# Kernel tuning notes

Measured on AMD Instinct MI355X. Metric: run time of the kernel, lower is better.

Reference implementation:

```python
import jax, jax.numpy as jnp
import numpy as np

GRID = (32, 32, 32)
LOWER = jnp.array([0.0, 0.0, 0.0], jnp.float32)
UPPER = jnp.array([1.0, 1.0, 1.0], jnp.float32)
B = 16
N = 131072
C_IN = 1018          # per-point feature channels; +3 offset +3 xyz = 1024 = nn_channels[0]
D_IN = 1024
C_OUT = 128          # nn_channels[-1]
BN_EPS = 1e-5


def setup_inputs() -> dict:
    key = jax.random.key(0)
    ks = jax.random.split(key, 8)
    W1 = jax.random.normal(ks[5], (D_IN, C_OUT), jnp.float32) / np.sqrt(D_IN).astype(np.float32)
    return {
        "xyz": jax.random.uniform(ks[0], (N, 3), jnp.float32),
        "pred_nocs": jax.random.uniform(ks[1], (N, 3), jnp.float32),
        "per_point_features": jax.random.normal(ks[2], (N, C_IN), jnp.float32),
        "pred_confidence": jax.random.uniform(ks[3], (N, 1), jnp.float32),
        "batch_idx": jnp.sort(jax.random.randint(ks[4], (N,), 0, B, dtype=jnp.int32)),
        "batch_size": B,
        "W1": W1,
        "b1": jnp.zeros((C_OUT,), jnp.float32),
        "g1": jnp.ones((C_OUT,), jnp.float32),
        "be1": jnp.zeros((C_OUT,), jnp.float32),
    }


def _batchnorm_train(x, gamma, beta):
    # torch BatchNorm1d in training mode: biased variance over the batch dim
    m = jnp.mean(x, axis=0)
    v = jnp.mean(jnp.square(x - m), axis=0)
    return (x - m) * jax.lax.rsqrt(v + BN_EPS) * gamma + beta


def reference(xyz, pred_nocs, per_point_features, pred_confidence, batch_idx,
              batch_size, W1, b1, g1, be1):
    gs_f = jnp.array(GRID, jnp.float32)
    gs_i = jnp.array(GRID, jnp.int32)
    # VirtualGrid.get_points_grid_idxs: round to nearest cell, clip into grid
    idx_f = jnp.round((pred_nocs - LOWER) / (UPPER - LOWER) * (gs_f - 1.0))
    idx = jnp.clip(idx_f.astype(jnp.int32), 0, gs_i - 1)  # [N,3]
    # VirtualGrid.idxs_to_points
    grid_pts = idx.astype(jnp.float32) / (gs_f - 1.0) * (UPPER - LOWER) + LOWER
    local_offset = pred_nocs - grid_pts
    feats = jnp.concatenate([per_point_features, local_offset, xyz], axis=-1)  # [N,1024]
    # local_nn: Linear -> ReLU -> PointBatchNorm1D
    h = _batchnorm_train(jax.nn.relu(feats @ W1 + b1), g1, be1)  # [N,128]
    # flatten (b,i,j,k) -> flat grid index
    gx, gy, gz = GRID
    flat = ((batch_idx.astype(jnp.int32) * gx + idx[:, 0]) * gy + idx[:, 1]) * gz + idx[:, 2]
    num_grids = batch_size * gx * gy * gz
    ssum = jax.ops.segment_sum(h, flat, num_segments=num_grids)          # [num_grids,128]
    cnt = jax.ops.segment_sum(jnp.ones((h.shape[0], 1), h.dtype), flat, num_segments=num_grids)
    mean = ssum / jnp.maximum(cnt, 1.0)  # empty cells stay 0 (torch_scatter mean)
    # [num_grids, C] -> [B, gx, gy, gz, C] -> [B, C, gx, gy, gz]
    vol = mean.reshape(batch_size, gx, gy, gz, C_OUT).transpose(0, 4, 1, 2, 3)
    return vol
```

## Files before the change

kernel.cpp:

```cpp
#include <hip/hip_runtime.h>

#define NPTS   131072
#define CIN    1018
#define DIN    1024
#define COUT   128
#define BB     16
#define GDIM   32
#define NCELLS (BB*GDIM*GDIM*GDIM)
#define NREP   8

typedef float          f32x4  __attribute__((ext_vector_type(4)));
typedef __bf16         bf16x8 __attribute__((ext_vector_type(8)));
typedef unsigned short us8    __attribute__((ext_vector_type(8)));

__device__ __forceinline__ unsigned short f2bf(float f) {
    union { float f; unsigned u; } v; v.f = f;
    unsigned r = v.u + 0x7FFFu + ((v.u >> 16) & 1u);
    return (unsigned short)(r >> 16);
}

__device__ __forceinline__ us8 cvt8f(f32x4 lo, f32x4 hi) {
    bf16x8 r;
    r[0] = (__bf16)lo[0]; r[1] = (__bf16)lo[1]; r[2] = (__bf16)lo[2]; r[3] = (__bf16)lo[3];
    r[4] = (__bf16)hi[0]; r[5] = (__bf16)hi[1]; r[6] = (__bf16)hi[2]; r[7] = (__bf16)hi[3];
    return __builtin_bit_cast(us8, r);
}

__device__ __forceinline__ f32x4 MF(us8 a, us8 b, f32x4 c) {
    return __builtin_amdgcn_mfma_f32_16x16x32_bf16(
        __builtin_bit_cast(bf16x8, a), __builtin_bit_cast(bf16x8, b), c, 0, 0, 0);
}

__global__ __launch_bounds__(256) void k_zero(int4* __restrict__ p, int n4) {
    const int idx = blockIdx.x * 256 + threadIdx.x;
    const int4 z = {0, 0, 0, 0};
    for (int i = idx; i < n4; i += 131072) p[i] = z;
}

__global__ __launch_bounds__(256) void k_packW(const float* __restrict__ W1,
                                               unsigned short* __restrict__ pw) {
    const int t  = blockIdx.x * 256 + threadIdx.x;
    const int l  = t & 63;
    const int cb = (t >> 6) & 7;
    const int ks = t >> 9;
    const int col  = cb * 16 + (l & 15);
    const int krow = ks * 32 + ((l >> 4) * 8);
    unsigned short* dst = pw + (size_t)t * 8;
#pragma unroll
    for (int i = 0; i < 8; ++i) dst[i] = f2bf(W1[(size_t)(krow + i) * COUT + col]);
}

__global__ __launch_bounds__(256) void k_prep(const float* __restrict__ xyz,
                                              const float* __restrict__ nocs,
                                              const float* __restrict__ feats,
                                              const int*   __restrict__ bidx,
                                              float* __restrict__ tail,
                                              int*   __restrict__ cellid,
                                              int*   __restrict__ cnt) {
    const int i = blockIdx.x * 256 + threadIdx.x;
    if (i >= NPTS) return;
    int id[3]; float off[3];
#pragma unroll
    for (int d = 0; d < 3; ++d) {
        const float nv = nocs[i * 3 + d];
        int ii = (int)rintf(nv * 31.0f);
        ii = ii < 0 ? 0 : (ii > 31 ? 31 : ii);
        id[d]  = ii;
        off[d] = nv - (float)ii / 31.0f;
    }
    float* tl = tail + (size_t)i * 8;
    tl[0] = feats[(size_t)i * CIN + 1016];
    tl[1] = feats[(size_t)i * CIN + 1017];
    tl[2] = off[0]; tl[3] = off[1]; tl[4] = off[2];
    tl[5] = xyz[i*3+0]; tl[6] = xyz[i*3+1]; tl[7] = xyz[i*3+2];
    const int cell = ((bidx[i] * GDIM + id[0]) * GDIM + id[1]) * GDIM + id[2];
    cellid[i] = cell;
    atomicAdd(&cnt[cell], 1);
}

__global__ __launch_bounds__(256) void k_scanA(const int* __restrict__ cnt,
                                               int* __restrict__ rel,
                                               int* __restrict__ bsum) {
    __shared__ int wtot[4], woff[4];
    const int t = threadIdx.x, blk = blockIdx.x;
    const int4 c4 = *(const int4*)&cnt[blk * 1024 + t * 4];
    const int s = c4.x + c4.y + c4.z + c4.w;
    int v = s;
    const int lane = t & 63, w = t >> 6;
#pragma unroll
    for (int d = 1; d < 64; d <<= 1) {
        const int u = __shfl_up(v, d);
        if (lane >= d) v += u;
    }
    if (lane == 63) wtot[w] = v;
    __syncthreads();
    if (t == 0) {
        int a = 0;
#pragma unroll
        for (int i = 0; i < 4; ++i) { woff[i] = a; a += wtot[i]; }
        bsum[blk] = a;
    }
    __syncthreads();
    const int excl = woff[w] + v - s;
    int* r = rel + blk * 1024 + t * 4;
    r[0] = excl; r[1] = excl + c4.x;
    r[2] = excl + c4.x + c4.y; r[3] = excl + c4.x + c4.y + c4.z;
}

__global__ __launch_bounds__(256) void k_scanB(const int* __restrict__ bsum,
                                               int* __restrict__ boff) {
    __shared__ int wtot[4], woff[4];
    const int t = threadIdx.x;
    const int2 c2 = *(const int2*)&bsum[t * 2];
    const int s = c2.x + c2.y;
    int v = s;
    const int lane = t & 63, w = t >> 6;
#pragma unroll
    for (int d = 1; d < 64; d <<= 1) {
        const int u = __shfl_up(v, d);
        if (lane >= d) v += u;
    }
    if (lane == 63) wtot[w] = v;
    __syncthreads();
    if (t == 0) {
        int a = 0;
#pragma unroll
        for (int i = 0; i < 4; ++i) { woff[i] = a; a += wtot[i]; }
    }
    __syncthreads();
    const int excl = woff[w] + v - s;
    boff[t * 2] = excl; boff[t * 2 + 1] = excl + c2.x;
}

__global__ __launch_bounds__(256) void k_fill(const int* __restrict__ cellid,
                                              const int* __restrict__ rel,
                                              const int* __restrict__ boff,
                                              int* __restrict__ cursor,
                                              int* __restrict__ dstrow) {
    const int i = blockIdx.x * 256 + threadIdx.x;
    if (i >= NPTS) return;
    const int cell = cellid[i];
    const int slot = atomicAdd(&cursor[cell], 1);
    dstrow[i] = rel[cell] + boff[cell >> 10] + slot;
}


template<int DIRECT>
__global__ void k_gemm(const float* __restrict__ feats,
                       const float* __restrict__ tail,
                       const int*   __restrict__ dstrow,
                       const float* __restrict__ b1,
                       const unsigned short* __restrict__ pw,
                       float* __restrict__ dst,
                       float* __restrict__ gstats) {
    __shared__ float S[3 * 12288];
    const int t = threadIdx.x;
    const int w = t >> 6, l = t & 63;
    const int kgrp = l >> 4, l15 = l & 15;
    const int row0b = blockIdx.x * 128;
    const int swz = l15 & 7;
    const int lr = w * 16 + l15;

    f32x4 acc[8];
#pragma unroll
    for (int cb = 0; cb < 8; ++cb) {
#pragma unroll
        for (int d = 0; d < 4; ++d) acc[cb][d] = 0.f;
    }

#define STAGE6(stg, ch) do{                                               \
    float* _base = S + (stg) * 12288;                                     \
    _Pragma("unroll")                                                     \
    for (int _i = 0; _i < 4; ++_i) {            \
        const int _s   = t + _i * 512;                                    \
        const int _row = _s >> 4;                                         \
        const int _c4  = (_s & 15) ^ (_row & 7);                          \
        const int _k   = (ch) * 64 + _c4 * 4;                             \
        const float* _src = (_k < 1016)                                   \
            ? feats + (size_t)(row0b + _row) * CIN + _k                   \
            : tail  + (size_t)(row0b + _row) * 8 + (_k - 1016);           \
        __builtin_amdgcn_global_load_lds(                                 \
            (const __attribute__((address_space(1))) void*)_src,          \
            (__attribute__((address_space(3))) void*)&_base[_s * 4],      \
            16, 0, 0);                                                    \
    }                                                                     \
    _Pragma("unroll")                                                     \
    for (int _i = 0; _i < 2; ++_i) {            \
        const int _s = t + _i * 512;                                      \
        __builtin_amdgcn_global_load_lds(                                 \
            (const __attribute__((address_space(1))) void*)                \
                (pw + (size_t)(ch) * 8192 + (size_t)_s * 8),              \
            (__attribute__((address_space(3))) void*)&_base[8192 + _s*4], \
            16, 0, 0);                                                    \
    }                                                                     \
}while(0)

    STAGE6(0, 0);
    STAGE6(1, 1);
    int cur = 0, nxt2 = 2;
    for (int ch = 0; ch < 16; ++ch) {
        __builtin_amdgcn_sched_barrier(0);
        if (ch == 15) asm volatile("s_waitcnt vmcnt(0)" ::: "memory");
        else          asm volatile("s_waitcnt vmcnt(6)" ::: "memory");
        __builtin_amdgcn_sched_barrier(0);
        __builtin_amdgcn_s_barrier();
        __builtin_amdgcn_sched_barrier(0);
        if (ch + 2 < 16) STAGE6(nxt2, ch + 2);
        const float* bufA = S + cur * 12288;
        const unsigned short* bufB = (const unsigned short*)(bufA + 8192);
#pragma unroll
        for (int ks = 0; ks < 2; ++ks) {
            const int c4a = ks * 8 + kgrp * 2;
            const f32x4 lo = *(const f32x4*)&bufA[lr * 64 + (( c4a      ^ swz) << 2)];
            const f32x4 hi = *(const f32x4*)&bufA[lr * 64 + (((c4a + 1) ^ swz) << 2)];
            const us8 a = cvt8f(lo, hi);
#pragma unroll
            for (int cb = 0; cb < 8; ++cb) {
                const us8 b = *(const us8*)(bufB + (((ks * 8 + cb) * 64) + l) * 8);
                acc[cb] = MF(a, b, acc[cb]);
            }
        }
        __builtin_amdgcn_sched_barrier(0);
        cur  = cur  == 2 ? 0 : cur + 1;
        nxt2 = nxt2 == 2 ? 0 : nxt2 + 1;
    }
#undef STAGE6

    int r0[4];
#pragma unroll
    for (int j = 0; j < 4; ++j)
        r0[j] = dstrow[row0b + w * 16 + kgrp * 4 + j];
    float* grep = gstats + (size_t)((blockIdx.x * 8 + w) & (NREP - 1)) * 256;
#pragma unroll
    for (int cb = 0; cb < 8; ++cb) {
        const int c = cb * 16 + l15;
        const float bias = b1[c];
        float s = 0.f, q = 0.f;
#pragma unroll
        for (int j = 0; j < 4; ++j) {
            float v0 = acc[cb][j] + bias; v0 = v0 > 0.f ? v0 : 0.f;
            if (DIRECT) {
                const int a = r0[j];
                unsafeAtomicAdd(dst + (((size_t)((a >> 15) * COUT + c)) << 15) + (a & 32767), v0);
            } else {
                dst[(size_t)r0[j] * COUT + c] = v0;
            }
            s += v0; q += v0 * v0;
        }
        s += __shfl_xor(s, 16); s += __shfl_xor(s, 32);
        q += __shfl_xor(q, 16); q += __shfl_xor(q, 32);
        if (l < 16) {
            unsafeAtomicAdd(grep + c, s);
            unsafeAtomicAdd(grep + COUT + c, q);
        }
    }
}

__global__ void k_stats(const float* __restrict__ gstats, const float* __restrict__ g1,
                        const float* __restrict__ be1, float* __restrict__ ss) {
    const int c = threadIdx.x;
    float sm = 0.f, sq = 0.f;
#pragma unroll
    for (int r = 0; r < NREP; ++r) {
        sm += gstats[r * 256 + c];
        sq += gstats[r * 256 + COUT + c];
    }
    const float invn = 1.0f / (float)NPTS;
    const float mean = sm * invn;
    float var = sq * invn - mean * mean;
    var = var < 0.f ? 0.f : var;
    const float sc = g1[c] * rsqrtf(var + 1e-5f);
    ss[c] = sc;
    ss[COUT + c] = be1[c] - mean * sc;
}

__global__ __launch_bounds__(256) void k_out(const float* __restrict__ h,
                                             const int* __restrict__ cnt,
                                             const int* __restrict__ rel,
                                             const int* __restrict__ boff,
                                             const float* __restrict__ ss,
                                             float* __restrict__ out) {
    __shared__ float tile[128 * 128];
    __shared__ float linv[128];
    __shared__ float lss[256];
    const int t  = threadIdx.x;
    const int s0 = blockIdx.x * 128;
    const int b = s0 >> 15, sp0 = s0 & 32767;
    const int boff0 = boff[s0 >> 10];
    if (t < 128) {
        const int cn = cnt[s0 + t];
        linv[t] = cn > 0 ? 1.0f / (float)cn : 0.f;
    } else {
        const int c = t - 128;
        lss[c] = ss[c]; lss[128 + c] = ss[COUT + c];
    }
    const int q = t & 31, r8 = t >> 5;
#pragma unroll
    for (int rep = 0; rep < 16; ++rep) {
        const int j = r8 + rep * 8;
        const int cj = cnt[s0 + j];
        if (cj > 0) {
            const int st = rel[s0 + j] + boff0;
            f32x4 v; v[0] = v[1] = v[2] = v[3] = 0.f;
            for (int k = 0; k < cj; ++k) {
                const f32x4 hv = *(const f32x4*)&h[(size_t)(st + k) * COUT + q * 4];
                v[0] += hv[0]; v[1] += hv[1]; v[2] += hv[2]; v[3] += hv[3];
            }
#pragma unroll
            for (int d = 0; d < 4; ++d) {
                const int c = q * 4 + d;
                tile[c * 128 + (j ^ (c & 28))] = v[d];
            }
        }
    }
    __syncthreads();
#pragma unroll
    for (int p = 0; p < 16; ++p) {
        const int c = p * 8 + r8;
        const float sc = lss[c], sh = lss[128 + c];
        const int u = c & 28;
        const f32x4 vv = *(const f32x4*)&tile[c * 128 + ((q * 4) ^ u)];
        f32x4 o;
#pragma unroll
        for (int d = 0; d < 4; ++d) {
            const float inv = linv[q * 4 + d];
            o[d] = inv > 0.f ? vv[d] * inv * sc + sh : 0.f;
        }
        *(f32x4*)&out[(((size_t)(b * COUT + c)) << 15) + sp0 + q * 4] = o;
    }
}

__global__ __launch_bounds__(256) void k_norm_inplace(float* __restrict__ out,
                                                      const int* __restrict__ cnt,
                                                      const float* __restrict__ ss,
                                                      size_t total) {
    const size_t i = ((size_t)blockIdx.x * 256 + threadIdx.x) * 4;
    if (i >= total) return;
    const int c = (int)((i >> 15) & 127);
    const size_t cellb = ((i >> 22) << 15) | (i & 32767);
    f32x4 v = *(f32x4*)&out[i];
    const int4 cn = *(const int4*)&cnt[cellb];
    const float sc = ss[c], sh = ss[COUT + c];
    const int cna[4] = {cn.x, cn.y, cn.z, cn.w};
#pragma unroll
    for (int d = 0; d < 4; ++d)
        v[d] = cna[d] > 0 ? v[d] / (float)cna[d] * sc + sh : 0.f;
    *(f32x4*)&out[i] = v;
}

extern "C" void kernel_launch(void* const* d_in, const int* in_sizes, int n_in,
                              void* d_out, int out_size, void* d_ws, size_t ws_size,
                              hipStream_t stream) {
    const float* xyz   = (const float*)d_in[0];
    const float* nocs  = (const float*)d_in[1];
    const float* feats = (const float*)d_in[2];
    const int*   bidx  = (const int*)d_in[4];
    const float* W1    = (const float*)d_in[6];
    const float* b1    = (const float*)d_in[7];
    const float* g1    = (const float*)d_in[8];
    const float* be1   = (const float*)d_in[9];
    float* out = (float*)d_out;
    float* ws  = (float*)d_ws;

    const size_t HF  = (size_t)NPTS * COUT;
    const size_t STF = NREP * 256;
    const size_t oA_h    = 0;
    const size_t oA_cnt  = HF;
    const size_t oA_cur  = oA_cnt + NCELLS;
    const size_t oA_st   = oA_cur + NCELLS;
    const size_t oA_rel  = oA_st + STF;
    const size_t oA_bof  = oA_rel + NCELLS;
    const size_t oA_dr   = oA_bof + 512;
    const size_t oA_ss   = oA_dr + NPTS;
    const size_t oA_tail = oA_ss + 256;
    const size_t oA_cid  = oA_tail + (size_t)NPTS * 8;
    const size_t oA_pw   = oA_cid + NPTS;
    const size_t needA   = (oA_pw + 65536) * sizeof(float);
    const bool planA = ws_size >= needA;

    const size_t oB_cnt = 0, oB_st = NCELLS, oB_ss = oB_st + STF,
                 oB_tail = oB_ss + 256, oB_cid = oB_tail + (size_t)NPTS * 8,
                 oB_pw = oB_cid + NPTS;

    float* h   = planA ? ws + oA_h : nullptr;
    int*   cnt = (int*)(ws + (planA ? oA_cnt : oB_cnt));
    int*   cur = planA ? (int*)(ws + oA_cur) : nullptr;
    float* st  = ws + (planA ? oA_st : oB_st);
    int*   rel = planA ? (int*)(ws + oA_rel) : nullptr;
    int*   bof = planA ? (int*)(ws + oA_bof) : nullptr;
    int*   dr  = planA ? (int*)(ws + oA_dr) : nullptr;
    float* ssb = ws + (planA ? oA_ss : oB_ss);
    float* tl  = ws + (planA ? oA_tail : oB_tail);
    int*   cid = (int*)(ws + (planA ? oA_cid : oB_cid));
    unsigned short* pw = (unsigned short*)(ws + (planA ? oA_pw : oB_pw));

    if (planA) {
        k_zero<<<512, 256, 0, stream>>>((int4*)cnt, (int)((2 * NCELLS + STF) / 4));
    } else {
        k_zero<<<512, 256, 0, stream>>>((int4*)cnt, (int)((NCELLS + STF) / 4));
        hipMemsetAsync(out, 0, (size_t)out_size * sizeof(float), stream);
    }

    k_packW<<<64, 256, 0, stream>>>(W1, pw);
    k_prep<<<NPTS / 256, 256, 0, stream>>>(xyz, nocs, feats, bidx, tl, cid, cnt);
    if (planA) {
        k_scanA<<<512, 256, 0, stream>>>(cnt, rel, bof);
        k_scanB<<<1, 256, 0, stream>>>(bof, bof);
        k_fill<<<NPTS / 256, 256, 0, stream>>>(cid, rel, bof, cur, dr);
        k_gemm<0><<<NPTS / 128, 512, 0, stream>>>(feats, tl, dr, b1, pw, h, st);
        k_stats<<<1, 128, 0, stream>>>(st, g1, be1, ssb);
        k_out<<<NCELLS / 128, 256, 0, stream>>>(h, cnt, rel, bof, ssb, out);
    } else {
        k_gemm<1><<<NPTS / 128, 512, 0, stream>>>(feats, tl, cid, b1, pw, out, st);
        k_stats<<<1, 128, 0, stream>>>(st, g1, be1, ssb);
        const size_t total = (size_t)out_size;
        k_norm_inplace<<<(unsigned)((total + 1023) / 1024), 256, 0, stream>>>(out, cnt, ssb, total);
    }
    (void)in_sizes; (void)n_in; (void)d_in;
}
```

Baseline: 346.6 us.

## Merge small launches, fold BN stats into output kernel, remap block order

Merges the weight-pack and zeroing kernels into one launch, moves cursor zeroing into the scan kernel, and folds the BN statistics reduction into each block of the output kernel so the single-block stats launch disappears. The GEMM and output kernels now use an XCD-aware block index remap. The output kernel is reshaped to 64 cells per block with a padded shared-memory tile instead of an XOR swizzle, which lowers LDS use and raises occupancy. The goal is less launch overhead and better cache locality, at the cost of every output block recomputing the stats reduction.

```diff
diff --git a/kernel.cpp b/kernel.cpp
--- a/kernel.cpp
+++ b/kernel.cpp
@@ -31,23 +31,25 @@
         __builtin_bit_cast(bf16x8, a), __builtin_bit_cast(bf16x8, b), c, 0, 0, 0);
 }
 
-__global__ __launch_bounds__(256) void k_zero(int4* __restrict__ p, int n4) {
-    const int idx = blockIdx.x * 256 + threadIdx.x;
-    const int4 z = {0, 0, 0, 0};
-    for (int i = idx; i < n4; i += 131072) p[i] = z;
-}
-
-__global__ __launch_bounds__(256) void k_packW(const float* __restrict__ W1,
-                                               unsigned short* __restrict__ pw) {
-    const int t  = blockIdx.x * 256 + threadIdx.x;
-    const int l  = t & 63;
-    const int cb = (t >> 6) & 7;
-    const int ks = t >> 9;
-    const int col  = cb * 16 + (l & 15);
-    const int krow = ks * 32 + ((l >> 4) * 8);
-    unsigned short* dst = pw + (size_t)t * 8;
-#pragma unroll
-    for (int i = 0; i < 8; ++i) dst[i] = f2bf(W1[(size_t)(krow + i) * COUT + col]);
+__global__ __launch_bounds__(256) void k_zp(const float* __restrict__ W1,
+                                            unsigned short* __restrict__ pw,
+                                            int4* __restrict__ zp, int n4) {
+    const int t = threadIdx.x;
+    if (blockIdx.x < 64) {
+        const int g  = blockIdx.x * 256 + t;
+        const int l  = g & 63;
+        const int cb = (g >> 6) & 7;
+        const int ks = g >> 9;
+        const int col  = cb * 16 + (l & 15);
+        const int krow = ks * 32 + ((l >> 4) * 8);
+        unsigned short* dst = pw + (size_t)g * 8;
+#pragma unroll
+        for (int i = 0; i < 8; ++i) dst[i] = f2bf(W1[(size_t)(krow + i) * COUT + col]);
+    } else {
+        const int idx = (blockIdx.x - 64) * 256 + t;
+        const int4 z = {0, 0, 0, 0};
+        for (int i = idx; i < n4; i += 512 * 256) zp[i] = z;
+    }
 }
 
 __global__ __launch_bounds__(256) void k_prep(const float* __restrict__ xyz,
@@ -80,9 +82,12 @@
 
 __global__ __launch_bounds__(256) void k_scanA(const int* __restrict__ cnt,
                                                int* __restrict__ rel,
-                                               int* __restrict__ bsum) {
+                                               int* __restrict__ bsum,
+                                               int4* __restrict__ cursor) {
     __shared__ int wtot[4], woff[4];
     const int t = threadIdx.x, blk = blockIdx.x;
+    const int4 z = {0, 0, 0, 0};
+    cursor[blk * 256 + t] = z;
     const int4 c4 = *(const int4*)&cnt[blk * 1024 + t * 4];
     const int s = c4.x + c4.y + c4.z + c4.w;
     int v = s;
@@ -157,7 +162,8 @@
     const int t = threadIdx.x;
     const int w = t >> 6, l = t & 63;
     const int kgrp = l >> 4, l15 = l & 15;
-    const int row0b = blockIdx.x * 128;
+    const int lb = (blockIdx.x & 7) * ((int)gridDim.x >> 3) + (blockIdx.x >> 3);
+    const int row0b = lb * 128;
     const int swz = l15 & 7;
     const int lr = w * 16 + l15;
 
@@ -278,25 +284,40 @@
                                              const int* __restrict__ cnt,
                                              const int* __restrict__ rel,
                                              const int* __restrict__ boff,
-                                             const float* __restrict__ ss,
+                                             const float* __restrict__ gstats,
+                                             const float* __restrict__ g1,
+                                             const float* __restrict__ be1,
                                              float* __restrict__ out) {
-    __shared__ float tile[128 * 128];
-    __shared__ float linv[128];
+    __shared__ float tile[128 * 68];
+    __shared__ float linv[64];
     __shared__ float lss[256];
     const int t  = threadIdx.x;
-    const int s0 = blockIdx.x * 128;
+    const int lb = (blockIdx.x & 7) * ((int)gridDim.x >> 3) + (blockIdx.x >> 3);
+    const int s0 = lb * 64;
     const int b = s0 >> 15, sp0 = s0 & 32767;
     const int boff0 = boff[s0 >> 10];
-    if (t < 128) {
+    if (t < 64) {
         const int cn = cnt[s0 + t];
         linv[t] = cn > 0 ? 1.0f / (float)cn : 0.f;
-    } else {
+    } else if (t >= 128) {
         const int c = t - 128;
-        lss[c] = ss[c]; lss[128 + c] = ss[COUT + c];
+        float sm = 0.f, sq = 0.f;
+#pragma unroll
+        for (int r = 0; r < NREP; ++r) {
+            sm += gstats[r * 256 + c];
+            sq += gstats[r * 256 + COUT + c];
+        }
+        const float invn = 1.0f / (float)NPTS;
+        const float mean = sm * invn;
+        float var = sq * invn - mean * mean;
+        var = var < 0.f ? 0.f : var;
+        const float sc = g1[c] * rsqrtf(var + 1e-5f);
+        lss[c] = sc;
+        lss[128 + c] = be1[c] - mean * sc;
     }
     const int q = t & 31, r8 = t >> 5;
 #pragma unroll
-    for (int rep = 0; rep < 16; ++rep) {
+    for (int rep = 0; rep < 8; ++rep) {
         const int j = r8 + rep * 8;
         const int cj = cnt[s0 + j];
         if (cj > 0) {
@@ -307,26 +328,23 @@
                 v[0] += hv[0]; v[1] += hv[1]; v[2] += hv[2]; v[3] += hv[3];
             }
 #pragma unroll
-            for (int d = 0; d < 4; ++d) {
-                const int c = q * 4 + d;
-                tile[c * 128 + (j ^ (c & 28))] = v[d];
-            }
+            for (int d = 0; d < 4; ++d) tile[(q * 4 + d) * 68 + j] = v[d];
         }
     }
     __syncthreads();
-#pragma unroll
-    for (int p = 0; p < 16; ++p) {
-        const int c = p * 8 + r8;
+    const int qq = t & 15, rr = t >> 4;
+#pragma unroll
+    for (int p = 0; p < 8; ++p) {
+        const int c = p * 16 + rr;
         const float sc = lss[c], sh = lss[128 + c];
-        const int u = c & 28;
-        const f32x4 vv = *(const f32x4*)&tile[c * 128 + ((q * 4) ^ u)];
+        const f32x4 vv = *(const f32x4*)&tile[c * 68 + qq * 4];
         f32x4 o;
 #pragma unroll
         for (int d = 0; d < 4; ++d) {
-            const float inv = linv[q * 4 + d];
+            const float inv = linv[qq * 4 + d];
             o[d] = inv > 0.f ? vv[d] * inv * sc + sh : 0.f;
         }
-        *(f32x4*)&out[(((size_t)(b * COUT + c)) << 15) + sp0 + q * 4] = o;
+        *(f32x4*)&out[(((size_t)(b * COUT + c)) << 15) + sp0 + qq * 4] = o;
     }
 }
 
@@ -366,9 +384,9 @@
     const size_t STF = NREP * 256;
     const size_t oA_h    = 0;
     const size_t oA_cnt  = HF;
-    const size_t oA_cur  = oA_cnt + NCELLS;
-    const size_t oA_st   = oA_cur + NCELLS;
-    const size_t oA_rel  = oA_st + STF;
+    const size_t oA_st   = oA_cnt + NCELLS;
+    const size_t oA_cur  = oA_st + STF;
+    const size_t oA_rel  = oA_cur + NCELLS;
     const size_t oA_bof  = oA_rel + NCELLS;
     const size_t oA_dr   = oA_bof + 512;
     const size_t oA_ss   = oA_dr + NPTS;
@@ -384,8 +402,8 @@
 
     float* h   = planA ? ws + oA_h : nullptr;
     int*   cnt = (int*)(ws + (planA ? oA_cnt : oB_cnt));
+    float* st  = ws + (planA ? oA_st : oB_st);
     int*   cur = planA ? (int*)(ws + oA_cur) : nullptr;
-    float* st  = ws + (planA ? oA_st : oB_st);
     int*   rel = planA ? (int*)(ws + oA_rel) : nullptr;
     int*   bof = planA ? (int*)(ws + oA_bof) : nullptr;
     int*   dr  = planA ? (int*)(ws + oA_dr) : nullptr;
@@ -394,22 +412,16 @@
     int*   cid = (int*)(ws + (planA ? oA_cid : oB_cid));
     unsigned short* pw = (unsigned short*)(ws + (planA ? oA_pw : oB_pw));
 
-    if (planA) {
-        k_zero<<<512, 256, 0, stream>>>((int4*)cnt, (int)((2 * NCELLS + STF) / 4));
-    } else {
-        k_zero<<<512, 256, 0, stream>>>((int4*)cnt, (int)((NCELLS + STF) / 4));
-        hipMemsetAsync(out, 0, (size_t)out_size * sizeof(float), stream);
-    }
-
-    k_packW<<<64, 256, 0, stream>>>(W1, pw);
+    k_zp<<<576, 256, 0, stream>>>(W1, pw, (int4*)cnt, (int)((NCELLS + STF) / 4));
+    if (!planA) hipMemsetAsync(out, 0, (size_t)out_size * sizeof(float), stream);
+
     k_prep<<<NPTS / 256, 256, 0, stream>>>(xyz, nocs, feats, bidx, tl, cid, cnt);
     if (planA) {
-        k_scanA<<<512, 256, 0, stream>>>(cnt, rel, bof);
+        k_scanA<<<512, 256, 0, stream>>>(cnt, rel, bof, (int4*)cur);
         k_scanB<<<1, 256, 0, stream>>>(bof, bof);
         k_fill<<<NPTS / 256, 256, 0, stream>>>(cid, rel, bof, cur, dr);
         k_gemm<0><<<NPTS / 128, 512, 0, stream>>>(feats, tl, dr, b1, pw, h, st);
-        k_stats<<<1, 128, 0, stream>>>(st, g1, be1, ssb);
-        k_out<<<NCELLS / 128, 256, 0, stream>>>(h, cnt, rel, bof, ssb, out);
+        k_out<<<NCELLS / 64, 256, 0, stream>>>(h, cnt, rel, bof, st, g1, be1, out);
     } else {
         k_gemm<1><<<NPTS / 128, 512, 0, stream>>>(feats, tl, cid, b1, pw, out, st);
         k_stats<<<1, 128, 0, stream>>>(st, g1, be1, ssb);
```

Measured after the change: 307.1 us, median of 2. 11.4% less time.
